# Kernel optimization log

Hardware: AMD Instinct MI355X
Metric: run time of the kernel (lower is better)

Reference implementation:

```python
import itertools
import jax, jax.numpy as jnp
import numpy as np

ALPHA = 1e-4   # mse/conn mixing
BETA = 0.1
DMAX = 20.0
NCAP = 10.0    # costs_n_cap
PCAP = 3.0     # costs_p_cap
W3D = 64       # 3D cube window (window_3d)
W2D = 32       # 2D MALIS window (window_2d, default)


def _dilate5(mask):
    # scipy binary_dilation, default cross structuring element, 5 iterations
    m = mask.astype(bool)
    for _ in range(5):
        p = np.pad(m, 1)
        m = p[1:-1, 1:-1] | p[:-2, 1:-1] | p[2:, 1:-1] | p[1:-1, :-2] | p[1:-1, 2:]
    return m


def _label8(mask):
    # skimage.measure.label on boolean mask: 8-connectivity, background=0
    H, W = mask.shape
    lbl = np.zeros((H, W), np.int64)
    parent = {}

    def find(x):
        while parent[x] != x:
            parent[x] = parent[parent[x]]
            x = parent[x]
        return x

    nxt = 1
    for i in range(H):
        for j in range(W):
            if not mask[i, j]:
                continue
            neigh = []
            for di, dj in ((-1, -1), (-1, 0), (-1, 1), (0, -1)):
                ii, jj = i + di, j + dj
                if 0 <= ii < H and 0 <= jj < W and mask[ii, jj]:
                    neigh.append(int(lbl[ii, jj]))
            if not neigh:
                lbl[i, j] = nxt
                parent[nxt] = nxt
                nxt += 1
            else:
                m0 = min(neigh)
                lbl[i, j] = m0
                for nb in neigh:
                    ra, rb = find(m0), find(nb)
                    if ra != rb:
                        parent[max(ra, rb)] = min(ra, rb)
    out = np.zeros_like(lbl)
    remap = {}
    c = 0
    for i in range(H):
        for j in range(W):
            if lbl[i, j] > 0:
                r = find(int(lbl[i, j]))
                if r not in remap:
                    c += 1
                    remap[r] = c
                out[i, j] = remap[r]
    return out


def _malis_edge_weights(seg, n1, n2, costs, pos):
    # MALIS union-find / Kruskal maximal-spanning-tree pair counting.
    # Edges processed in descending cost order. Background (seg==0) nodes
    # are not counted. pos=1: #same-label pairs merged; pos=0: #diff-label pairs.
    n = seg.size
    parent = list(range(n))

    def find(x):
        r = x
        while parent[r] != r:
            r = parent[r]
        while parent[x] != r:
            parent[x], x = r, parent[x]
        return r

    cnt = [({int(s): 1} if s > 0 else {}) for s in seg]
    tot = [1 if s > 0 else 0 for s in seg]
    w = np.zeros(costs.shape[0], np.float32)
    for e in np.argsort(-costs, kind="stable"):
        ra, rb = find(int(n1[e])), find(int(n2[e]))
        if ra == rb:
            continue
        ca, cb = cnt[ra], cnt[rb]
        if len(ca) > len(cb):
            ra, rb, ca, cb = rb, ra, cb, ca
        same = 0
        for l, v in ca.items():
            same += v * cb.get(l, 0)
        w[e] = float(same if pos else tot[ra] * tot[rb] - same)
        for l, v in ca.items():
            cb[l] = cb.get(l, 0) + v
        tot[rb] += tot[ra]
        parent[ra] = rb
        cnt[ra] = None
    return w


def _window_weights(pred2d, tgt2d):
    # numpy MALIS node weights for a [B,1,H,W] 2D projection
    B, C, H, W = pred2d.shape
    w = W2D
    wn = np.zeros(pred2d.shape, np.float32)
    wp = np.zeros(pred2d.shape, np.float32)
    idx = np.arange(w * w).reshape(w, w)
    n1 = np.concatenate([idx[:, :-1].ravel(), idx[:-1, :].ravel()])
    n2 = np.concatenate([idx[:, 1:].ravel(), idx[1:, :].ravel()])
    nh = w * (w - 1)
    for k in range(H // w):
        for j in range(W // w):
            p = pred2d[:, :, k*w:(k+1)*w, j*w:(j+1)*w]
            t = tgt2d[:, :, k*w:(k+1)*w, j*w:(j+1)*w]
            ch = (p[:, :, :, :-1] + p[:, :, :, 1:]).reshape(B, -1)
            cv = (p[:, :, :-1, :] + p[:, :, 1:, :]).reshape(B, -1)
            costs = np.concatenate([ch, cv], 1).astype(np.float32)
            gh = (t[:, :, :, :-1] + t[:, :, :, 1:]).reshape(B, -1)
            gv = (t[:, :, :-1, :] + t[:, :, 1:, :]).reshape(B, -1)
            gt = np.concatenate([gh, gv], 1).astype(np.float32)
            costs_n = costs.copy()
            costs_p = costs.copy()
            costs_n[gt > NCAP] = NCAP
            costs_p[gt < PCAP] = 0.0
            gt = np.minimum(gt, NCAP)
            for b in range(B):
                sg = _label8(~_dilate5(t[b, 0] == 0)).ravel()
                en = _malis_edge_weights(sg, n1, n2, costs_n[b], 0)
                ep = _malis_edge_weights(sg, n1, n2, costs_p[b], 1)
                sn = en.sum()
                if sn > 0:
                    en = en / sn
                sp = ep.sum()
                if sp > 0:
                    ep = ep / sp
                en[gt[b] >= PCAP] = 0.0
                ep[gt[b] < NCAP] = 0.0
                for ew, out in ((en, wn), (ep, wp)):
                    eh = ew[:nh].reshape(w, w - 1)
                    ev = ew[nh:].reshape(w - 1, w)
                    nwt = np.zeros((w, w), np.float32)
                    nwt[:, :-1] += eh
                    nwt[:, 1:] += eh
                    nwt[:-1, :] += ev
                    nwt[1:, :] += ev
                    out[b, 0, k*w:(k+1)*w, j*w:(j+1)*w] = nwt
    return wn, wp


def _precompute(pred_np, tgt_np):
    # host-side (detached) MALIS weight maps, exactly as the torch module
    B, C, H, W, D = pred_np.shape
    items = []
    for k, j, i in itertools.product(range(H // W3D), range(W // W3D), range(D // W3D)):
        sl = (slice(None), slice(None), slice(k*W3D, (k+1)*W3D),
              slice(j*W3D, (j+1)*W3D), slice(i*W3D, (i+1)*W3D))
        pc, tc = pred_np[sl], tgt_np[sl]
        for axis in (2, 3, 4):
            wn, wp = _window_weights(pc.min(axis=axis), tc.min(axis=axis))
            items.append((k, j, i, axis, jnp.asarray(wn), jnp.asarray(wp)))
    return items


def _loss(pred, target, items):
    mse = jnp.mean((pred - target) ** 2)
    conn = jnp.float32(0.0)
    for (k, j, i, axis, wn, wp) in items:
        pc = pred[:, :, k*W3D:(k+1)*W3D, j*W3D:(j+1)*W3D, i*W3D:(i+1)*W3D]
        proj = jnp.min(pc, axis=axis)  # [B,1,64,64]
        conn = conn + jnp.sum(proj**2 * wn + BETA * (DMAX - proj)**2 * wp)
    return (mse, jnp.float32(ALPHA) * conn)


def setup_inputs() -> dict:
    # synthetic distance-transform-like volumes (zeros on 'vessel' seeds)
    rng = np.random.default_rng(0)
    B, H = 4, 128
    g = np.arange(H, dtype=np.float32)
    zz, yy, xx = np.meshgrid(g, g, g, indexing="ij")
    tgt = np.empty((B, 1, H, H, H), np.float32)
    for b in range(B):
        pts = rng.uniform(0, H, size=(24, 3)).astype(np.float32)
        d = np.full((H, H, H), np.inf, np.float32)
        for p in pts:
            d = np.minimum(d, np.sqrt((zz - p[0])**2 + (yy - p[1])**2 + (xx - p[2])**2))
        tgt[b, 0] = np.floor(np.minimum(d, DMAX))
    pred = np.clip(tgt + 0.5 * rng.standard_normal(tgt.shape).astype(np.float32), 0.0, DMAX).astype(np.float32)
    return {"pred": jnp.asarray(pred), "target": jnp.asarray(tgt)}


def reference(pred, target):
    items = _precompute(np.asarray(pred), np.asarray(target))
    return _loss(pred, target, items)
```

## Files before the change

### kernel.cpp

```cpp
#include <hip/hip_runtime.h>

#define BLOCK 256
#define NNODE 1024
#define NH    992
#define NE    1984
#define NSORT 2048
#define LMAX  12
#define CHUNK 64
#define NPASS (NE / CHUNK)

typedef unsigned long long ull;

__device__ __forceinline__ void edge_nodes(int e, int& a, int& b) {
    if (e < NH) {
        int r = e / 31;
        int c = e - r * 31;
        a = (r << 5) + c;
        b = a + 1;
    } else {
        a = e - NH;
        b = a + 32;
    }
}

__device__ __forceinline__ int find_par(unsigned short* par, int x) {
    volatile unsigned short* vp = par;
    int r = x;
    int p = vp[r];
    while (p != r) { r = p; p = vp[r]; }
    int c = x;
    while (c != r) { const int nxt = vp[c]; vp[c] = (unsigned short)r; c = nxt; }
    return r;
}

__device__ __forceinline__ int dot16x4(ull a, ull b) {
    int s  = (int)(a & 0xFFFFu)         * (int)(b & 0xFFFFu);
    s     += (int)((a >> 16) & 0xFFFFu) * (int)((b >> 16) & 0xFFFFu);
    s     += (int)((a >> 32) & 0xFFFFu) * (int)((b >> 32) & 0xFFFFu);
    s     += (int)((a >> 48) & 0xFFFFu) * (int)((b >> 48) & 0xFFFFu);
    return s;
}

__device__ __forceinline__ void cswap(unsigned int& ka, unsigned short& ia,
                                      unsigned int& kb, unsigned short& ib, bool up) {
    const bool gt = (ka > kb) || (ka == kb && ia > ib);
    if (gt == up) {
        const unsigned int  tk = ka; ka = kb; kb = tk;
        const unsigned short ti = ia; ia = ib; ib = ti;
    }
}

template<int MODE>
__device__ __forceinline__ void kruskal_run(unsigned short* sh_parent,
                                            unsigned int*   sh_szto,
                                            ull*            sh_cnt64,
                                            unsigned int*   sh_key,
                                            const unsigned short* sh_idx,
                                            const int sign, const int lane) {
    unsigned int* claim32 = (unsigned int*)sh_cnt64;
    for (int pass = 0; pass < NPASS; ++pass) {
        const int e = sh_idx[pass * CHUNK + lane];
        int a, bb; edge_nodes(e, a, bb);
        int ra = find_par(sh_parent, a);
        int rb = find_par(sh_parent, bb);
        bool cand = (ra != rb);

        if (MODE <= 1) {
            const unsigned int tag = ((unsigned int)(pass + 1) << 6) | (unsigned int)(63 - lane);
            const int ia = (MODE == 0) ? ra : (ra * 6 + 2);
            const int ib = (MODE == 0) ? rb : (rb * 6 + 2);
            if (cand) {
                atomicMax(&claim32[ia], tag);
                atomicMax(&claim32[ib], tag);
            }
            asm volatile("s_waitcnt lgkmcnt(0)" ::: "memory");
            __builtin_amdgcn_sched_barrier(0);
            bool win = false;
            if (cand) win = (claim32[ia] == tag) && (claim32[ib] == tag);
            if (win) {
                const unsigned int xa = sh_szto[ra], xb = sh_szto[rb];
                const int ta = (int)(xa >> 16), tb = (int)(xb >> 16);
                int wv;
                ull a0 = 0, b0 = 0;
                if (MODE == 0) {
                    wv = ta * tb;
                } else {
                    a0 = sh_cnt64[ra * 3]; b0 = sh_cnt64[rb * 3];
                    const int same = dot16x4(a0, b0);
                    wv = sign ? same : (ta * tb - same);
                }
                const int big = ((xa & 0xFFFFu) > (xb & 0xFFFFu));
                const int rs = big ? ra : rb;
                const int rl = big ? rb : ra;
                sh_key[e] = __float_as_uint((float)wv);
                sh_szto[rs] = xa + xb;
                if (MODE == 1 && (ta + tb) > 0) sh_cnt64[rs * 3] = a0 + b0;
                sh_parent[rl] = (unsigned short)rs;
                cand = false;
            }
            asm volatile("s_waitcnt lgkmcnt(0)" ::: "memory");
            __builtin_amdgcn_sched_barrier(0);
            if (cand) {
                ra = find_par(sh_parent, ra);
                rb = find_par(sh_parent, rb);
                cand = (ra != rb);
            }
        }

        ull m = __ballot(cand);
        while (m) {
            const int i = (int)__builtin_ctzll(m);
            m &= m - 1;
            const unsigned int pack = (unsigned int)ra | ((unsigned int)rb << 10) | ((unsigned int)e << 20);
            const unsigned int pk = (unsigned int)__shfl((int)pack, i);
            const int ra_i = (int)(pk & 1023u);
            const int rb_i = (int)((pk >> 10) & 1023u);
            if (ra_i == rb_i) continue;
            const int se = (int)(pk >> 20);
            const unsigned int xa = sh_szto[ra_i], xb = sh_szto[rb_i];
            const int ta = (int)(xa >> 16), tb = (int)(xb >> 16);
            const int big = ((xa & 0xFFFFu) > (xb & 0xFFFFu));
            const int rs = big ? ra_i : rb_i;
            const int rl = big ? rb_i : ra_i;
            int wv;
            if (MODE == 0) {
                wv = ta * tb;
            } else if (MODE == 1) {
                const ull a0 = sh_cnt64[ra_i * 3];
                const ull b0 = sh_cnt64[rb_i * 3];
                const int same = dot16x4(a0, b0);
                wv = sign ? same : (ta * tb - same);
                if (lane == 0 && (ta + tb) > 0)
                    sh_cnt64[rs * 3] = a0 + b0;
            } else {
                const ull a0 = sh_cnt64[ra_i * 3 + 0];
                const ull a1 = sh_cnt64[ra_i * 3 + 1];
                const ull a2 = sh_cnt64[ra_i * 3 + 2];
                const ull b0 = sh_cnt64[rb_i * 3 + 0];
                const ull b1 = sh_cnt64[rb_i * 3 + 1];
                const ull b2 = sh_cnt64[rb_i * 3 + 2];
                const int same = dot16x4(a0, b0) + dot16x4(a1, b1) + dot16x4(a2, b2);
                wv = sign ? same : (ta * tb - same);
                if (lane == 0 && (ta + tb) > 0) {
                    sh_cnt64[rs * 3 + 0] = a0 + b0;
                    sh_cnt64[rs * 3 + 1] = a1 + b1;
                    sh_cnt64[rs * 3 + 2] = a2 + b2;
                }
            }
            if (lane == 0) {
                sh_key[se] = __float_as_uint((float)wv);
                sh_szto[rs] = xa + xb;
                sh_parent[rl] = (unsigned short)rs;
            }
            if (ra == rl) ra = rs;
            if (rb == rl) rb = rs;
        }
    }
}

template<int MODE>
__device__ __forceinline__ void uf_init(unsigned short* sh_parent,
                                        unsigned int* sh_szto,
                                        ull* sh_cnt64,
                                        const unsigned char* sh_seg,
                                        const int tid) {
    unsigned int* claim32 = (unsigned int*)sh_cnt64;
    for (int pix = tid; pix < NNODE; pix += BLOCK) {
        sh_parent[pix] = (unsigned short)pix;
        const int s = sh_seg[pix];
        const unsigned int tot = (s > 0 && s <= LMAX) ? 1u : 0u;
        sh_szto[pix] = 1u | (tot << 16);
        if (MODE == 0) {
            claim32[pix] = 0u;
        } else {
            ull c0 = 0, c1 = 0, c2 = 0;
            if (s >= 1 && s <= LMAX) {
                const ull bit = 1ull << (((s - 1) & 3) * 16);
                const int q = (s - 1) >> 2;
                if (q == 0) c0 = bit; else if (q == 1) c1 = bit; else c2 = bit;
            }
            sh_cnt64[pix * 3 + 0] = c0;
            sh_cnt64[pix * 3 + 1] = (MODE == 1) ? 0ull : c1;
            if (MODE == 2) sh_cnt64[pix * 3 + 2] = c2;
        }
    }
}

__global__ __launch_bounds__(BLOCK) void prep_kernel(const float* __restrict__ pred,
                                                     const float* __restrict__ tgt,
                                                     char* __restrict__ ws,
                                                     double* __restrict__ acc_ws,
                                                     int B) {
    __shared__ alignas(16) float sh_p[NNODE];
    __shared__ alignas(16) float sh_t[NNODE];
    __shared__ unsigned char  mA[NNODE];
    __shared__ unsigned char  mB[NNODE];
    __shared__ unsigned short sh_parent[NNODE];
    __shared__ unsigned short sh_lab[NNODE];
    __shared__ int sh_flag;
    __shared__ int sh_L;
    __shared__ double sh_redp[4];

    const int tid = threadIdx.x;
    const int w = blockIdx.x;
    int wg = w;
    const int b    = wg % B;  wg /= B;
    const int win  = wg & 3;  wg >>= 2;
    const int item = wg;
    const int axis_id = item % 3;
    const int cube = item / 3;
    const int ci = cube & 1;
    const int cj = (cube >> 1) & 1;
    const int ck = (cube >> 2) & 1;
    const int wk = win >> 1;
    const int wj = win & 1;

    const int NW = 96 * B;
    float* Pb = (float*)(ws + 64);
    float* Tb = Pb + (size_t)NW * NNODE;
    unsigned char* Sb = (unsigned char*)(Tb + (size_t)NW * NNODE);
    int* Lb = (int*)(Sb + (size_t)NW * NNODE);

    const size_t base = (size_t)b * 2097152u;

    if (axis_id == 2) {
        double msum = 0.0;
        for (int pix = tid; pix < NNODE; pix += BLOCK) {
            const int r = pix >> 5, c = pix & 31;
            const int R = wk * 32 + r, C = wj * 32 + c;
            const size_t idx0 = base + (size_t)(ck * 64 + R) * 16384u + (size_t)(cj * 64 + C) * 128u + (size_t)(ci * 64);
            const float4* pp = reinterpret_cast<const float4*>(pred + idx0);
            const float4* tp = reinterpret_cast<const float4*>(tgt + idx0);
            float pm = 3.4e38f, tm = 3.4e38f;
            #pragma unroll
            for (int h = 0; h < 16; ++h) {
                const float4 a = pp[h];
                const float4 t = tp[h];
                pm = fminf(pm, fminf(fminf(a.x, a.y), fminf(a.z, a.w)));
                tm = fminf(tm, fminf(fminf(t.x, t.y), fminf(t.z, t.w)));
                const float dx = a.x - t.x, dy = a.y - t.y;
                const float dz = a.z - t.z, dw = a.w - t.w;
                msum += (double)(dx * dx);
                msum += (double)(dy * dy);
                msum += (double)(dz * dz);
                msum += (double)(dw * dw);
            }
            sh_p[pix] = pm;
            sh_t[pix] = tm;
        }
        for (int off = 32; off > 0; off >>= 1) msum += __shfl_down(msum, off, 64);
        if ((tid & 63) == 0) sh_redp[tid >> 6] = msum;
        __syncthreads();
        if (tid == 0)
            atomicAdd(&acc_ws[0], sh_redp[0] + sh_redp[1] + sh_redp[2] + sh_redp[3]);
    } else {
        const int r  = tid >> 3;
        const int c0 = (tid & 7) << 2;
        const int R = wk * 32 + r, C = wj * 32 + c0;
        size_t idx0; int hstride;
        if (axis_id == 0) {
            idx0 = base + (size_t)(ck * 64) * 16384u + (size_t)(cj * 64 + R) * 128u + (size_t)(ci * 64 + C);
            hstride = 16384;
        } else {
            idx0 = base + (size_t)(ck * 64 + R) * 16384u + (size_t)(cj * 64) * 128u + (size_t)(ci * 64 + C);
            hstride = 128;
        }
        float4 pm = make_float4(3.4e38f, 3.4e38f, 3.4e38f, 3.4e38f);
        float4 tm = pm;
        #pragma unroll 8
        for (int h = 0; h < 64; ++h) {
            const float4 a  = *reinterpret_cast<const float4*>(pred + idx0);
            const float4 t4 = *reinterpret_cast<const float4*>(tgt + idx0);
            pm.x = fminf(pm.x, a.x);  pm.y = fminf(pm.y, a.y);
            pm.z = fminf(pm.z, a.z);  pm.w = fminf(pm.w, a.w);
            tm.x = fminf(tm.x, t4.x); tm.y = fminf(tm.y, t4.y);
            tm.z = fminf(tm.z, t4.z); tm.w = fminf(tm.w, t4.w);
            idx0 += (size_t)hstride;
        }
        *reinterpret_cast<float4*>(&sh_p[(r << 5) + c0]) = pm;
        *reinterpret_cast<float4*>(&sh_t[(r << 5) + c0]) = tm;
        __syncthreads();
    }

    for (int pix = tid; pix < NNODE; pix += BLOCK)
        mA[pix] = (sh_t[pix] == 0.0f) ? 1 : 0;
    __syncthreads();
    for (int it = 0; it < 5; ++it) {
        unsigned char* src = (it & 1) ? mB : mA;
        unsigned char* dst = (it & 1) ? mA : mB;
        for (int pix = tid; pix < NNODE; pix += BLOCK) {
            const int r = pix >> 5, c = pix & 31;
            unsigned char v = src[pix];
            if (r > 0)  v |= src[pix - 32];
            if (r < 31) v |= src[pix + 32];
            if (c > 0)  v |= src[pix - 1];
            if (c < 31) v |= src[pix + 1];
            dst[pix] = v;
        }
        __syncthreads();
    }
    for (int pix = tid; pix < NNODE; pix += BLOCK)
        mA[pix] = mB[pix] ^ 1;
    __syncthreads();

    for (int pix = tid; pix < NNODE; pix += BLOCK)
        sh_parent[pix] = mA[pix] ? (unsigned short)pix : (unsigned short)0xFFFF;
    __syncthreads();
    for (;;) {
        if (tid == 0) sh_flag = 0;
        __syncthreads();
        for (int pix = tid; pix < NNODE; pix += BLOCK) {
            if (!mA[pix]) continue;
            const int r = pix >> 5, c = pix & 31;
            int m = sh_parent[pix];
            #pragma unroll
            for (int d = 0; d < 8; ++d) {
                static const int dr[8] = {-1,-1,-1, 0, 0, 1, 1, 1};
                static const int dc[8] = {-1, 0, 1,-1, 1,-1, 0, 1};
                const int rr = r + dr[d], cc = c + dc[d];
                if (rr < 0 || rr > 31 || cc < 0 || cc > 31) continue;
                const int nb = (rr << 5) + cc;
                if (mA[nb]) { int v = sh_parent[nb]; if (v < m) m = v; }
            }
            while ((int)sh_parent[m] < m) m = sh_parent[m];
            if (m < (int)sh_parent[pix]) { sh_parent[pix] = (unsigned short)m; sh_flag = 1; }
        }
        __syncthreads();
        const int f = sh_flag;
        __syncthreads();
        if (f == 0) break;
    }

    if (tid == 0) sh_L = 0;
    __syncthreads();
    for (int pix = tid; pix < NNODE; pix += BLOCK) {
        if (mA[pix] && (int)sh_parent[pix] == pix) {
            const int id = atomicAdd(&sh_L, 1);
            sh_lab[pix] = (unsigned short)(id + 1);
        }
    }
    __syncthreads();

    {
        const int p4 = tid << 2;
        *reinterpret_cast<float4*>(&Pb[(size_t)w * NNODE + p4]) =
            *reinterpret_cast<const float4*>(&sh_p[p4]);
        *reinterpret_cast<float4*>(&Tb[(size_t)w * NNODE + p4]) =
            *reinterpret_cast<const float4*>(&sh_t[p4]);
        unsigned int packed = 0;
        #pragma unroll
        for (int q = 0; q < 4; ++q) {
            const int pix = p4 + q;
            unsigned int s = 0;
            if (mA[pix]) {
                int lab = sh_lab[sh_parent[pix]];
                if (lab > 255) lab = 255;
                s = (unsigned int)lab;
            }
            packed |= s << (q * 8);
        }
        ((unsigned int*)Sb)[(size_t)w * (NNODE / 4) + tid] = packed;
        if (tid == 0) Lb[w] = sh_L;
    }
}

__global__ __launch_bounds__(BLOCK) void solve_kernel(const char* __restrict__ ws_c,
                                                      double* __restrict__ acc_ws,
                                                      int B) {
    __shared__ alignas(16) float          sh_p[NNODE];
    __shared__ alignas(16) float          sh_t[NNODE];
    __shared__ alignas(16) unsigned int   sh_key[NSORT];
    __shared__ alignas(16) unsigned short sh_idx[NSORT];
    __shared__ unsigned short sh_parent[NNODE];
    __shared__ unsigned int   sh_szto[NNODE];
    __shared__ ull            sh_cnt64[NNODE * 3];
    __shared__ alignas(16) unsigned char sh_seg[NNODE];
    __shared__ float          sh_sn;
    __shared__ double         sh_red[4];

    const int tid = threadIdx.x;
    int wg = blockIdx.x;
    const int sign = wg & 1;  wg >>= 1;
    const int w = wg;

    const int NW = 96 * B;
    const float* Pb = (const float*)(ws_c + 64);
    const float* Tb = Pb + (size_t)NW * NNODE;
    const unsigned char* Sb = (const unsigned char*)(Tb + (size_t)NW * NNODE);
    const int* Lb = (const int*)(Sb + (size_t)NW * NNODE);

    const int Lraw = Lb[w];
    if (Lraw == 0 || (Lraw == 1 && sign == 0)) return;
    const int mode = (Lraw <= 1) ? 0 : ((Lraw <= 4) ? 1 : 2);

    {
        const int p4 = tid << 2;
        *reinterpret_cast<float4*>(&sh_p[p4]) =
            *reinterpret_cast<const float4*>(&Pb[(size_t)w * NNODE + p4]);
        *reinterpret_cast<float4*>(&sh_t[p4]) =
            *reinterpret_cast<const float4*>(&Tb[(size_t)w * NNODE + p4]);
        ((unsigned int*)sh_seg)[tid] =
            ((const unsigned int*)Sb)[(size_t)w * (NNODE / 4) + tid];
    }
    __syncthreads();

    if (mode == 0)      uf_init<0>(sh_parent, sh_szto, sh_cnt64, sh_seg, tid);
    else if (mode == 1) uf_init<1>(sh_parent, sh_szto, sh_cnt64, sh_seg, tid);
    else                uf_init<2>(sh_parent, sh_szto, sh_cnt64, sh_seg, tid);
    __syncthreads();

    unsigned int   K[8];
    unsigned short I[8];
    const int b8 = tid << 3;
    #pragma unroll
    for (int l = 0; l < 8; ++l) {
        const int e = b8 + l;
        if (e < NE) {
            int a, bb; edge_nodes(e, a, bb);
            float cost = sh_p[a] + sh_p[bb];
            const float g = sh_t[a] + sh_t[bb];
            if (sign == 0) { if (g > 10.0f) cost = 10.0f; }
            else           { if (g <  3.0f) cost = 0.0f;  }
            K[l] = ~__float_as_uint(cost);
            I[l] = (unsigned short)e;
        } else {
            K[l] = 0xFFFFFFFFu;
            I[l] = (unsigned short)0xFFFF;
        }
    }
    cswap(K[0],I[0],K[1],I[1], true );
    cswap(K[2],I[2],K[3],I[3], false);
    cswap(K[4],I[4],K[5],I[5], true );
    cswap(K[6],I[6],K[7],I[7], false);
    cswap(K[0],I[0],K[2],I[2], true );
    cswap(K[1],I[1],K[3],I[3], true );
    cswap(K[4],I[4],K[6],I[6], false);
    cswap(K[5],I[5],K[7],I[7], false);
    cswap(K[0],I[0],K[1],I[1], true );
    cswap(K[2],I[2],K[3],I[3], true );
    cswap(K[4],I[4],K[5],I[5], false);
    cswap(K[6],I[6],K[7],I[7], false);
    {
        const bool u8 = ((b8 & 8) == 0);
        cswap(K[0],I[0],K[4],I[4], u8); cswap(K[1],I[1],K[5],I[5], u8);
        cswap(K[2],I[2],K[6],I[6], u8); cswap(K[3],I[3],K[7],I[7], u8);
        cswap(K[0],I[0],K[2],I[2], u8); cswap(K[1],I[1],K[3],I[3], u8);
        cswap(K[4],I[4],K[6],I[6], u8); cswap(K[5],I[5],K[7],I[7], u8);
        cswap(K[0],I[0],K[1],I[1], u8); cswap(K[2],I[2],K[3],I[3], u8);
        cswap(K[4],I[4],K[5],I[5], u8); cswap(K[6],I[6],K[7],I[7], u8);
    }
    {
        uint4 k0, k1, iv;
        k0.x=K[0]; k0.y=K[1]; k0.z=K[2]; k0.w=K[3];
        k1.x=K[4]; k1.y=K[5]; k1.z=K[6]; k1.w=K[7];
        iv.x=(unsigned int)I[0] | ((unsigned int)I[1]<<16);
        iv.y=(unsigned int)I[2] | ((unsigned int)I[3]<<16);
        iv.z=(unsigned int)I[4] | ((unsigned int)I[5]<<16);
        iv.w=(unsigned int)I[6] | ((unsigned int)I[7]<<16);
        *reinterpret_cast<uint4*>(&sh_key[b8])     = k0;
        *reinterpret_cast<uint4*>(&sh_key[b8 + 4]) = k1;
        *reinterpret_cast<uint4*>(&sh_idx[b8])     = iv;
    }
    __syncthreads();

    for (int k = 16; k <= NSORT; k <<= 1) {
        for (int j = k >> 1; j >= 8; j >>= 1) {
            for (int p = tid; p < (NSORT >> 1); p += BLOCK) {
                const int i   = ((p & ~(j - 1)) << 1) | (p & (j - 1));
                const int ixj = i | j;
                const unsigned int ka = sh_key[i], kb = sh_key[ixj];
                const unsigned short ia = sh_idx[i], ib = sh_idx[ixj];
                const bool gt = (ka > kb) || (ka == kb && ia > ib);
                const bool up = ((i & k) == 0);
                if (gt == up) {
                    sh_key[i] = kb; sh_key[ixj] = ka;
                    sh_idx[i] = ib; sh_idx[ixj] = ia;
                }
            }
            __syncthreads();
        }
        {
            const uint4 k0 = *reinterpret_cast<const uint4*>(&sh_key[b8]);
            const uint4 k1 = *reinterpret_cast<const uint4*>(&sh_key[b8 + 4]);
            const uint4 iv = *reinterpret_cast<const uint4*>(&sh_idx[b8]);
            K[0]=k0.x; K[1]=k0.y; K[2]=k0.z; K[3]=k0.w;
            K[4]=k1.x; K[5]=k1.y; K[6]=k1.z; K[7]=k1.w;
            I[0]=(unsigned short)(iv.x); I[1]=(unsigned short)(iv.x>>16);
            I[2]=(unsigned short)(iv.y); I[3]=(unsigned short)(iv.y>>16);
            I[4]=(unsigned short)(iv.z); I[5]=(unsigned short)(iv.z>>16);
            I[6]=(unsigned short)(iv.w); I[7]=(unsigned short)(iv.w>>16);
            const bool u8 = ((b8 & k) == 0);
            cswap(K[0],I[0],K[4],I[4], u8); cswap(K[1],I[1],K[5],I[5], u8);
            cswap(K[2],I[2],K[6],I[6], u8); cswap(K[3],I[3],K[7],I[7], u8);
            cswap(K[0],I[0],K[2],I[2], u8); cswap(K[1],I[1],K[3],I[3], u8);
            cswap(K[4],I[4],K[6],I[6], u8); cswap(K[5],I[5],K[7],I[7], u8);
            cswap(K[0],I[0],K[1],I[1], u8); cswap(K[2],I[2],K[3],I[3], u8);
            cswap(K[4],I[4],K[5],I[5], u8); cswap(K[6],I[6],K[7],I[7], u8);
            uint4 o0, o1, ov;
            o0.x=K[0]; o0.y=K[1]; o0.z=K[2]; o0.w=K[3];
            o1.x=K[4]; o1.y=K[5]; o1.z=K[6]; o1.w=K[7];
            ov.x=(unsigned int)I[0] | ((unsigned int)I[1]<<16);
            ov.y=(unsigned int)I[2] | ((unsigned int)I[3]<<16);
            ov.z=(unsigned int)I[4] | ((unsigned int)I[5]<<16);
            ov.w=(unsigned int)I[6] | ((unsigned int)I[7]<<16);
            *reinterpret_cast<uint4*>(&sh_key[b8])     = o0;
            *reinterpret_cast<uint4*>(&sh_key[b8 + 4]) = o1;
            *reinterpret_cast<uint4*>(&sh_idx[b8])     = ov;
        }
        __syncthreads();
    }

    for (int e = tid; e < NE; e += BLOCK) sh_key[e] = 0u;
    __syncthreads();

    if (tid < 64) {
        if (mode == 0)      kruskal_run<0>(sh_parent, sh_szto, sh_cnt64, sh_key, sh_idx, sign, tid);
        else if (mode == 1) kruskal_run<1>(sh_parent, sh_szto, sh_cnt64, sh_key, sh_idx, sign, tid);
        else                kruskal_run<2>(sh_parent, sh_szto, sh_cnt64, sh_key, sh_idx, sign, tid);
    }
    __syncthreads();

    {
        float part = 0.0f;
        for (int e = tid; e < NE; e += BLOCK) part += __uint_as_float(sh_key[e]);
        for (int off = 32; off > 0; off >>= 1) part += __shfl_down(part, off, 64);
        if ((tid & 63) == 0) sh_red[tid >> 6] = (double)part;
        __syncthreads();
        if (tid == 0) sh_sn = (float)(sh_red[0] + sh_red[1] + sh_red[2] + sh_red[3]);
        __syncthreads();
    }
    const float sn = sh_sn;

    double acc = 0.0;
    for (int pix = tid; pix < NNODE; pix += BLOCK) {
        const int r = pix >> 5, c = pix & 31;
        float nw = 0.0f;
        if (c < 31) { const int e = r * 31 + c;
            float v = __uint_as_float(sh_key[e]); if (sn > 0.0f) v = v / sn;
            const float g = sh_t[pix] + sh_t[pix + 1];
            if (sign == 0) { if (g >= 3.0f) v = 0.0f; } else { if (g < 10.0f) v = 0.0f; }
            nw += v; }
        if (c > 0)  { const int e = r * 31 + c - 1;
            float v = __uint_as_float(sh_key[e]); if (sn > 0.0f) v = v / sn;
            const float g = sh_t[pix - 1] + sh_t[pix];
            if (sign == 0) { if (g >= 3.0f) v = 0.0f; } else { if (g < 10.0f) v = 0.0f; }
            nw += v; }
        if (r < 31) { const int e = NH + pix;
            float v = __uint_as_float(sh_key[e]); if (sn > 0.0f) v = v / sn;
            const float g = sh_t[pix] + sh_t[pix + 32];
            if (sign == 0) { if (g >= 3.0f) v = 0.0f; } else { if (g < 10.0f) v = 0.0f; }
            nw += v; }
        if (r > 0)  { const int e = NH + pix - 32;
            float v = __uint_as_float(sh_key[e]); if (sn > 0.0f) v = v / sn;
            const float g = sh_t[pix - 32] + sh_t[pix];
            if (sign == 0) { if (g >= 3.0f) v = 0.0f; } else { if (g < 10.0f) v = 0.0f; }
            nw += v; }
        const float p = sh_p[pix];
        float term;
        if (sign == 0) term = (p * p) * nw;
        else { const float d = 20.0f - p; term = (0.1f * (d * d)) * nw; }
        acc += (double)term;
    }
    for (int off = 32; off > 0; off >>= 1) acc += __shfl_down(acc, off, 64);
    if ((tid & 63) == 0) sh_red[tid >> 6] = acc;
    __syncthreads();
    if (tid == 0)
        atomicAdd(&acc_ws[1], sh_red[0] + sh_red[1] + sh_red[2] + sh_red[3]);
}

__global__ __launch_bounds__(BLOCK) void conn_kernel(const float* __restrict__ pred,
                                                     const float* __restrict__ tgt,
                                                     double* __restrict__ acc_ws,
                                                     int B) {
    __shared__ alignas(16) float          sh_p[NNODE];
    __shared__ alignas(16) float          sh_t[NNODE];
    __shared__ alignas(16) unsigned int   sh_key[NSORT];
    __shared__ alignas(16) unsigned short sh_idx[NSORT];
    __shared__ unsigned short sh_parent[NNODE];
    __shared__ unsigned int   sh_szto[NNODE];
    __shared__ ull            sh_cnt64[NNODE * 3];
    __shared__ unsigned char  sh_seg[NNODE];
    __shared__ int            sh_flag;
    __shared__ int            sh_L;
    __shared__ float          sh_sn;
    __shared__ double         sh_red[4];

    const int tid = threadIdx.x;
    int wg = blockIdx.x;
    const int sign = (wg >> 3) & 1;
    wg = (wg & 7) | ((wg >> 4) << 3);
    const int b    = wg % B;  wg /= B;
    const int win  = wg & 3;  wg >>= 2;
    const int item = wg;
    const int axis_id = item % 3;
    const int cube = item / 3;
    const int ci = cube & 1;
    const int cj = (cube >> 1) & 1;
    const int ck = (cube >> 2) & 1;
    const int wk = win >> 1;
    const int wj = win & 1;

    const size_t base = (size_t)b * 2097152u;

    if (axis_id == 2) {
        for (int pix = tid; pix < NNODE; pix += BLOCK) {
            const int r = pix >> 5, c = pix & 31;
            const int R = wk * 32 + r, C = wj * 32 + c;
            const size_t idx0 = base + (size_t)(ck * 64 + R) * 16384u + (size_t)(cj * 64 + C) * 128u + (size_t)(ci * 64);
            const float4* pp = reinterpret_cast<const float4*>(pred + idx0);
            const float4* tp = reinterpret_cast<const float4*>(tgt + idx0);
            float pm = 3.4e38f, tm = 3.4e38f;
            #pragma unroll
            for (int h = 0; h < 16; ++h) {
                const float4 a = pp[h];
                const float4 t = tp[h];
                pm = fminf(pm, fminf(fminf(a.x, a.y), fminf(a.z, a.w)));
                tm = fminf(tm, fminf(fminf(t.x, t.y), fminf(t.z, t.w)));
            }
            sh_p[pix] = pm;
            sh_t[pix] = tm;
        }
    } else {
        const int r  = tid >> 3;
        const int c0 = (tid & 7) << 2;
        const int R = wk * 32 + r, C = wj * 32 + c0;
        size_t idx0; int hstride;
        if (axis_id == 0) {
            idx0 = base + (size_t)(ck * 64) * 16384u + (size_t)(cj * 64 + R) * 128u + (size_t)(ci * 64 + C);
            hstride = 16384;
        } else {
            idx0 = base + (size_t)(ck * 64 + R) * 16384u + (size_t)(cj * 64) * 128u + (size_t)(ci * 64 + C);
            hstride = 128;
        }
        float4 pm = make_float4(3.4e38f, 3.4e38f, 3.4e38f, 3.4e38f);
        float4 tm = pm;
        #pragma unroll 8
        for (int h = 0; h < 64; ++h) {
            const float4 a  = *reinterpret_cast<const float4*>(pred + idx0);
            const float4 t4 = *reinterpret_cast<const float4*>(tgt + idx0);
            pm.x = fminf(pm.x, a.x);  pm.y = fminf(pm.y, a.y);
            pm.z = fminf(pm.z, a.z);  pm.w = fminf(pm.w, a.w);
            tm.x = fminf(tm.x, t4.x); tm.y = fminf(tm.y, t4.y);
            tm.z = fminf(tm.z, t4.z); tm.w = fminf(tm.w, t4.w);
            idx0 += (size_t)hstride;
        }
        *reinterpret_cast<float4*>(&sh_p[(r << 5) + c0]) = pm;
        *reinterpret_cast<float4*>(&sh_t[(r << 5) + c0]) = tm;
    }
    __syncthreads();

    unsigned char* mA = sh_seg;
    unsigned char* mB = (unsigned char*)sh_idx;
    for (int pix = tid; pix < NNODE; pix += BLOCK)
        mA[pix] = (sh_t[pix] == 0.0f) ? 1 : 0;
    __syncthreads();
    for (int it = 0; it < 5; ++it) {
        unsigned char* src = (it & 1) ? mB : mA;
        unsigned char* dst = (it & 1) ? mA : mB;
        for (int pix = tid; pix < NNODE; pix += BLOCK) {
            const int r = pix >> 5, c = pix & 31;
            unsigned char v = src[pix];
            if (r > 0)  v |= src[pix - 32];
            if (r < 31) v |= src[pix + 32];
            if (c > 0)  v |= src[pix - 1];
            if (c < 31) v |= src[pix + 1];
            dst[pix] = v;
        }
        __syncthreads();
    }
    for (int pix = tid; pix < NNODE; pix += BLOCK)
        mA[pix] = mB[pix] ^ 1;
    __syncthreads();

    for (int pix = tid; pix < NNODE; pix += BLOCK)
        sh_parent[pix] = mA[pix] ? (unsigned short)pix : (unsigned short)0xFFFF;
    __syncthreads();
    for (;;) {
        if (tid == 0) sh_flag = 0;
        __syncthreads();
        for (int pix = tid; pix < NNODE; pix += BLOCK) {
            if (!mA[pix]) continue;
            const int r = pix >> 5, c = pix & 31;
            int m = sh_parent[pix];
            #pragma unroll
            for (int d = 0; d < 8; ++d) {
                static const int dr[8] = {-1,-1,-1, 0, 0, 1, 1, 1};
                static const int dc[8] = {-1, 0, 1,-1, 1,-1, 0, 1};
                const int rr = r + dr[d], cc = c + dc[d];
                if (rr < 0 || rr > 31 || cc < 0 || cc > 31) continue;
                const int nb = (rr << 5) + cc;
                if (mA[nb]) { int v = sh_parent[nb]; if (v < m) m = v; }
            }
            while ((int)sh_parent[m] < m) m = sh_parent[m];
            if (m < (int)sh_parent[pix]) { sh_parent[pix] = (unsigned short)m; sh_flag = 1; }
        }
        __syncthreads();
        const int f = sh_flag;
        __syncthreads();
        if (f == 0) break;
    }

    if (tid == 0) sh_L = 0;
    __syncthreads();
    for (int pix = tid; pix < NNODE; pix += BLOCK) {
        if (mA[pix] && (int)sh_parent[pix] == pix) {
            const int id = atomicAdd(&sh_L, 1);
            sh_szto[pix] = (unsigned int)(id + 1);
        }
    }
    __syncthreads();
    for (int pix = tid; pix < NNODE; pix += BLOCK) {
        unsigned char s = 0;
        if (mA[pix]) {
            int lab = (int)sh_szto[sh_parent[pix]];
            if (lab > 255) lab = 255;
            s = (unsigned char)lab;
        }
        sh_seg[pix] = s;
    }
    __syncthreads();

    const int Lraw = sh_L;
    const int mode = (Lraw <= 1) ? 0 : ((Lraw <= 4) ? 1 : 2);
    const bool skip_all = (Lraw == 0) || (Lraw == 1 && sign == 0);

    if (!skip_all) {

    if (mode == 0)      uf_init<0>(sh_parent, sh_szto, sh_cnt64, sh_seg, tid);
    else if (mode == 1) uf_init<1>(sh_parent, sh_szto, sh_cnt64, sh_seg, tid);
    else                uf_init<2>(sh_parent, sh_szto, sh_cnt64, sh_seg, tid);
    __syncthreads();

    unsigned int   K[8];
    unsigned short I[8];
    const int b8 = tid << 3;
    #pragma unroll
    for (int l = 0; l < 8; ++l) {
        const int e = b8 + l;
        if (e < NE) {
            int a, bb; edge_nodes(e, a, bb);
            float cost = sh_p[a] + sh_p[bb];
            const float g = sh_t[a] + sh_t[bb];
            if (sign == 0) { if (g > 10.0f) cost = 10.0f; }
            else           { if (g <  3.0f) cost = 0.0f;  }
            K[l] = ~__float_as_uint(cost);
            I[l] = (unsigned short)e;
        } else {
            K[l] = 0xFFFFFFFFu;
            I[l] = (unsigned short)0xFFFF;
        }
    }
    cswap(K[0],I[0],K[1],I[1], true );
    cswap(K[2],I[2],K[3],I[3], false);
    cswap(K[4],I[4],K[5],I[5], true );
    cswap(K[6],I[6],K[7],I[7], false);
    cswap(K[0],I[0],K[2],I[2], true );
    cswap(K[1],I[1],K[3],I[3], true );
    cswap(K[4],I[4],K[6],I[6], false);
    cswap(K[5],I[5],K[7],I[7], false);
    cswap(K[0],I[0],K[1],I[1], true );
    cswap(K[2],I[2],K[3],I[3], true );
    cswap(K[4],I[4],K[5],I[5], false);
    cswap(K[6],I[6],K[7],I[7], false);
    {
        const bool u8 = ((b8 & 8) == 0);
        cswap(K[0],I[0],K[4],I[4], u8); cswap(K[1],I[1],K[5],I[5], u8);
        cswap(K[2],I[2],K[6],I[6], u8); cswap(K[3],I[3],K[7],I[7], u8);
        cswap(K[0],I[0],K[2],I[2], u8); cswap(K[1],I[1],K[3],I[3], u8);
        cswap(K[4],I[4],K[6],I[6], u8); cswap(K[5],I[5],K[7],I[7], u8);
        cswap(K[0],I[0],K[1],I[1], u8); cswap(K[2],I[2],K[3],I[3], u8);
        cswap(K[4],I[4],K[5],I[5], u8); cswap(K[6],I[6],K[7],I[7], u8);
    }
    {
        uint4 k0, k1, iv;
        k0.x=K[0]; k0.y=K[1]; k0.z=K[2]; k0.w=K[3];
        k1.x=K[4]; k1.y=K[5]; k1.z=K[6]; k1.w=K[7];
        iv.x=(unsigned int)I[0] | ((unsigned int)I[1]<<16);
        iv.y=(unsigned int)I[2] | ((unsigned int)I[3]<<16);
        iv.z=(unsigned int)I[4] | ((unsigned int)I[5]<<16);
        iv.w=(unsigned int)I[6] | ((unsigned int)I[7]<<16);
        *reinterpret_cast<uint4*>(&sh_key[b8])     = k0;
        *reinterpret_cast<uint4*>(&sh_key[b8 + 4]) = k1;
        *reinterpret_cast<uint4*>(&sh_idx[b8])     = iv;
    }
    __syncthreads();

    for (int k = 16; k <= NSORT; k <<= 1) {
        for (int j = k >> 1; j >= 8; j >>= 1) {
            for (int p = tid; p < (NSORT >> 1); p += BLOCK) {
                const int i   = ((p & ~(j - 1)) << 1) | (p & (j - 1));
                const int ixj = i | j;
                const unsigned int ka = sh_key[i], kb = sh_key[ixj];
                const unsigned short ia = sh_idx[i], ib = sh_idx[ixj];
                const bool gt = (ka > kb) || (ka == kb && ia > ib);
                const bool up = ((i & k) == 0);
                if (gt == up) {
                    sh_key[i] = kb; sh_key[ixj] = ka;
                    sh_idx[i] = ib; sh_idx[ixj] = ia;
                }
            }
            __syncthreads();
        }
        {
            const uint4 k0 = *reinterpret_cast<const uint4*>(&sh_key[b8]);
            const uint4 k1 = *reinterpret_cast<const uint4*>(&sh_key[b8 + 4]);
            const uint4 iv = *reinterpret_cast<const uint4*>(&sh_idx[b8]);
            K[0]=k0.x; K[1]=k0.y; K[2]=k0.z; K[3]=k0.w;
            K[4]=k1.x; K[5]=k1.y; K[6]=k1.z; K[7]=k1.w;
            I[0]=(unsigned short)(iv.x); I[1]=(unsigned short)(iv.x>>16);
            I[2]=(unsigned short)(iv.y); I[3]=(unsigned short)(iv.y>>16);
            I[4]=(unsigned short)(iv.z); I[5]=(unsigned short)(iv.z>>16);
            I[6]=(unsigned short)(iv.w); I[7]=(unsigned short)(iv.w>>16);
            const bool u8 = ((b8 & k) == 0);
            cswap(K[0],I[0],K[4],I[4], u8); cswap(K[1],I[1],K[5],I[5], u8);
            cswap(K[2],I[2],K[6],I[6], u8); cswap(K[3],I[3],K[7],I[7], u8);
            cswap(K[0],I[0],K[2],I[2], u8); cswap(K[1],I[1],K[3],I[3], u8);
            cswap(K[4],I[4],K[6],I[6], u8); cswap(K[5],I[5],K[7],I[7], u8);
            cswap(K[0],I[0],K[1],I[1], u8); cswap(K[2],I[2],K[3],I[3], u8);
            cswap(K[4],I[4],K[5],I[5], u8); cswap(K[6],I[6],K[7],I[7], u8);
            uint4 o0, o1, ov;
            o0.x=K[0]; o0.y=K[1]; o0.z=K[2]; o0.w=K[3];
            o1.x=K[4]; o1.y=K[5]; o1.z=K[6]; o1.w=K[7];
            ov.x=(unsigned int)I[0] | ((unsigned int)I[1]<<16);
            ov.y=(unsigned int)I[2] | ((unsigned int)I[3]<<16);
            ov.z=(unsigned int)I[4] | ((unsigned int)I[5]<<16);
            ov.w=(unsigned int)I[6] | ((unsigned int)I[7]<<16);
            *reinterpret_cast<uint4*>(&sh_key[b8])     = o0;
            *reinterpret_cast<uint4*>(&sh_key[b8 + 4]) = o1;
            *reinterpret_cast<uint4*>(&sh_idx[b8])     = ov;
        }
        __syncthreads();
    }

    for (int e = tid; e < NE; e += BLOCK) sh_key[e] = 0u;
    __syncthreads();

    if (tid < 64) {
        if (mode == 0)      kruskal_run<0>(sh_parent, sh_szto, sh_cnt64, sh_key, sh_idx, sign, tid);
        else if (mode == 1) kruskal_run<1>(sh_parent, sh_szto, sh_cnt64, sh_key, sh_idx, sign, tid);
        else                kruskal_run<2>(sh_parent, sh_szto, sh_cnt64, sh_key, sh_idx, sign, tid);
    }
    __syncthreads();

    {
        float part = 0.0f;
        for (int e = tid; e < NE; e += BLOCK) part += __uint_as_float(sh_key[e]);
        for (int off = 32; off > 0; off >>= 1) part += __shfl_down(part, off, 64);
        if ((tid & 63) == 0) sh_red[tid >> 6] = (double)part;
        __syncthreads();
        if (tid == 0) sh_sn = (float)(sh_red[0] + sh_red[1] + sh_red[2] + sh_red[3]);
        __syncthreads();
    }
    const float sn = sh_sn;

    double acc = 0.0;
    for (int pix = tid; pix < NNODE; pix += BLOCK) {
        const int r = pix >> 5, c = pix & 31;
        float nw = 0.0f;
        if (c < 31) { const int e = r * 31 + c;
            float v = __uint_as_float(sh_key[e]); if (sn > 0.0f) v = v / sn;
            const float g = sh_t[pix] + sh_t[pix + 1];
            if (sign == 0) { if (g >= 3.0f) v = 0.0f; } else { if (g < 10.0f) v = 0.0f; }
            nw += v; }
        if (c > 0)  { const int e = r * 31 + c - 1;
            float v = __uint_as_float(sh_key[e]); if (sn > 0.0f) v = v / sn;
            const float g = sh_t[pix - 1] + sh_t[pix];
            if (sign == 0) { if (g >= 3.0f) v = 0.0f; } else { if (g < 10.0f) v = 0.0f; }
            nw += v; }
        if (r < 31) { const int e = NH + pix;
            float v = __uint_as_float(sh_key[e]); if (sn > 0.0f) v = v / sn;
            const float g = sh_t[pix] + sh_t[pix + 32];
            if (sign == 0) { if (g >= 3.0f) v = 0.0f; } else { if (g < 10.0f) v = 0.0f; }
            nw += v; }
        if (r > 0)  { const int e = NH + pix - 32;
            float v = __uint_as_float(sh_key[e]); if (sn > 0.0f) v = v / sn;
            const float g = sh_t[pix - 32] + sh_t[pix];
            if (sign == 0) { if (g >= 3.0f) v = 0.0f; } else { if (g < 10.0f) v = 0.0f; }
            nw += v; }
        const float p = sh_p[pix];
        float term;
        if (sign == 0) term = (p * p) * nw;
        else { const float d = 20.0f - p; term = (0.1f * (d * d)) * nw; }
        acc += (double)term;
    }
    for (int off = 32; off > 0; off >>= 1) acc += __shfl_down(acc, off, 64);
    if ((tid & 63) == 0) sh_red[tid >> 6] = acc;
    __syncthreads();
    if (tid == 0)
        atomicAdd(&acc_ws[1], sh_red[0] + sh_red[1] + sh_red[2] + sh_red[3]);

    }
}

__global__ __launch_bounds__(BLOCK) void mse_kernel(const float* __restrict__ pred,
                                                    const float* __restrict__ tgt,
                                                    double* __restrict__ acc_ws,
                                                    long n) {
    double acc = 0.0;
    for (long i = (long)blockIdx.x * BLOCK + threadIdx.x; i < n; i += (long)gridDim.x * BLOCK) {
        const float d = pred[i] - tgt[i];
        acc += (double)(d * d);
    }
    for (int off = 32; off > 0; off >>= 1) acc += __shfl_down(acc, off, 64);
    __shared__ double red[4];
    if ((threadIdx.x & 63) == 0) red[threadIdx.x >> 6] = acc;
    __syncthreads();
    if (threadIdx.x == 0)
        atomicAdd(&acc_ws[0], red[0] + red[1] + red[2] + red[3]);
}

__global__ void fin_kernel(const double* __restrict__ acc_ws, float* __restrict__ out, long n) {
    if (threadIdx.x == 0 && blockIdx.x == 0) {
        out[0] = (float)(acc_ws[0] / (double)n);
        out[1] = (float)(acc_ws[1] * (double)1e-4f);
    }
}

extern "C" void kernel_launch(void* const* d_in, const int* in_sizes, int n_in,
                              void* d_out, int out_size, void* d_ws, size_t ws_size,
                              hipStream_t stream) {
    const float* pred = (const float*)d_in[0];
    const float* tgt  = (const float*)d_in[1];
    float* out = (float*)d_out;
    double* acc = (double*)d_ws;

    const long n = (long)in_sizes[0];
    const int  B = (int)(n / 2097152);
    const int  NW = 96 * B;
    const size_t need = 64 + (size_t)NW * NNODE * 9 + (size_t)NW * 4;

    hipMemsetAsync(d_ws, 0, 2 * sizeof(double), stream);
    if (ws_size >= need) {
        prep_kernel<<<NW, BLOCK, 0, stream>>>(pred, tgt, (char*)d_ws, acc, B);
        solve_kernel<<<192 * B, BLOCK, 0, stream>>>((const char*)d_ws, acc, B);
    } else {
        mse_kernel<<<1024, BLOCK, 0, stream>>>(pred, tgt, acc, n);
        conn_kernel<<<192 * B, BLOCK, 0, stream>>>(pred, tgt, acc, B);
    }
    fin_kernel<<<1, 64, 0, stream>>>(acc, out, n);
}
```

Baseline: 473.4 us.

## Extend parallel claim-based Kruskal merging to more label counts with repeated rounds

The parallel atomicMax claim phase of the wave-level Kruskal pass now also runs for windows with up to 8 labels, using the spare third slot of each node's count array as the claim word. It also repeats the claim/merge step up to three rounds per 64-edge chunk, stopping early once fewer than 10 candidates remain. A new mode 3 keeps the old fully serial path for windows with more than 8 labels. The aim is to shrink the serial ballot loop, which handles one merge per iteration. The cost is extra atomics, LDS traffic and find calls per round, and more template instantiations.

```diff
diff --git a/kernel.cpp b/kernel.cpp
--- a/kernel.cpp
+++ b/kernel.cpp
@@ -65,45 +65,57 @@
         int rb = find_par(sh_parent, bb);
         bool cand = (ra != rb);
 
-        if (MODE <= 1) {
-            const unsigned int tag = ((unsigned int)(pass + 1) << 6) | (unsigned int)(63 - lane);
-            const int ia = (MODE == 0) ? ra : (ra * 6 + 2);
-            const int ib = (MODE == 0) ? rb : (rb * 6 + 2);
-            if (cand) {
-                atomicMax(&claim32[ia], tag);
-                atomicMax(&claim32[ib], tag);
-            }
-            asm volatile("s_waitcnt lgkmcnt(0)" ::: "memory");
-            __builtin_amdgcn_sched_barrier(0);
-            bool win = false;
-            if (cand) win = (claim32[ia] == tag) && (claim32[ib] == tag);
-            if (win) {
-                const unsigned int xa = sh_szto[ra], xb = sh_szto[rb];
-                const int ta = (int)(xa >> 16), tb = (int)(xb >> 16);
-                int wv;
-                ull a0 = 0, b0 = 0;
-                if (MODE == 0) {
-                    wv = ta * tb;
-                } else {
-                    a0 = sh_cnt64[ra * 3]; b0 = sh_cnt64[rb * 3];
-                    const int same = dot16x4(a0, b0);
-                    wv = sign ? same : (ta * tb - same);
+        if (MODE < 3) {
+            for (int round = 0; round < 3; ++round) {
+                const unsigned int tag =
+                    ((unsigned int)(pass * 4 + round + 1) << 6) | (unsigned int)(63 - lane);
+                const int ia = ra * 6 + 2 * MODE;
+                const int ib = rb * 6 + 2 * MODE;
+                if (cand) {
+                    atomicMax(&claim32[ia], tag);
+                    atomicMax(&claim32[ib], tag);
                 }
-                const int big = ((xa & 0xFFFFu) > (xb & 0xFFFFu));
-                const int rs = big ? ra : rb;
-                const int rl = big ? rb : ra;
-                sh_key[e] = __float_as_uint((float)wv);
-                sh_szto[rs] = xa + xb;
-                if (MODE == 1 && (ta + tb) > 0) sh_cnt64[rs * 3] = a0 + b0;
-                sh_parent[rl] = (unsigned short)rs;
-                cand = false;
-            }
-            asm volatile("s_waitcnt lgkmcnt(0)" ::: "memory");
-            __builtin_amdgcn_sched_barrier(0);
-            if (cand) {
-                ra = find_par(sh_parent, ra);
-                rb = find_par(sh_parent, rb);
-                cand = (ra != rb);
+                asm volatile("s_waitcnt lgkmcnt(0)" ::: "memory");
+                __builtin_amdgcn_sched_barrier(0);
+                bool win = false;
+                if (cand) win = (claim32[ia] == tag) && (claim32[ib] == tag);
+                if (win) {
+                    const unsigned int xa = sh_szto[ra], xb = sh_szto[rb];
+                    const int ta = (int)(xa >> 16), tb = (int)(xb >> 16);
+                    int wv;
+                    ull a0 = 0, a1 = 0, b0 = 0, b1 = 0;
+                    if (MODE == 0) {
+                        wv = ta * tb;
+                    } else {
+                        a0 = sh_cnt64[ra * 3]; b0 = sh_cnt64[rb * 3];
+                        int same = dot16x4(a0, b0);
+                        if (MODE >= 2) {
+                            a1 = sh_cnt64[ra * 3 + 1]; b1 = sh_cnt64[rb * 3 + 1];
+                            same += dot16x4(a1, b1);
+                        }
+                        wv = sign ? same : (ta * tb - same);
+                    }
+                    const int big = ((xa & 0xFFFFu) > (xb & 0xFFFFu));
+                    const int rs = big ? ra : rb;
+                    const int rl = big ? rb : ra;
+                    sh_key[e] = __float_as_uint((float)wv);
+                    sh_szto[rs] = xa + xb;
+                    if (MODE >= 1 && (ta + tb) > 0) {
+                        sh_cnt64[rs * 3] = a0 + b0;
+                        if (MODE >= 2) sh_cnt64[rs * 3 + 1] = a1 + b1;
+                    }
+                    sh_parent[rl] = (unsigned short)rs;
+                    cand = false;
+                }
+                asm volatile("s_waitcnt lgkmcnt(0)" ::: "memory");
+                __builtin_amdgcn_sched_barrier(0);
+                if (cand) {
+                    ra = find_par(sh_parent, ra);
+                    rb = find_par(sh_parent, rb);
+                    cand = (ra != rb);
+                }
+                const ull P = __ballot(cand);
+                if (__popcll(P) < 10) break;
             }
         }
 
@@ -125,26 +137,24 @@
             int wv;
             if (MODE == 0) {
                 wv = ta * tb;
-            } else if (MODE == 1) {
-                const ull a0 = sh_cnt64[ra_i * 3];
-                const ull b0 = sh_cnt64[rb_i * 3];
-                const int same = dot16x4(a0, b0);
-                wv = sign ? same : (ta * tb - same);
-                if (lane == 0 && (ta + tb) > 0)
-                    sh_cnt64[rs * 3] = a0 + b0;
             } else {
                 const ull a0 = sh_cnt64[ra_i * 3 + 0];
-                const ull a1 = sh_cnt64[ra_i * 3 + 1];
-                const ull a2 = sh_cnt64[ra_i * 3 + 2];
                 const ull b0 = sh_cnt64[rb_i * 3 + 0];
-                const ull b1 = sh_cnt64[rb_i * 3 + 1];
-                const ull b2 = sh_cnt64[rb_i * 3 + 2];
-                const int same = dot16x4(a0, b0) + dot16x4(a1, b1) + dot16x4(a2, b2);
+                ull a1 = 0, a2 = 0, b1 = 0, b2 = 0;
+                int same = dot16x4(a0, b0);
+                if (MODE >= 2) {
+                    a1 = sh_cnt64[ra_i * 3 + 1]; b1 = sh_cnt64[rb_i * 3 + 1];
+                    same += dot16x4(a1, b1);
+                }
+                if (MODE >= 3) {
+                    a2 = sh_cnt64[ra_i * 3 + 2]; b2 = sh_cnt64[rb_i * 3 + 2];
+                    same += dot16x4(a2, b2);
+                }
                 wv = sign ? same : (ta * tb - same);
                 if (lane == 0 && (ta + tb) > 0) {
                     sh_cnt64[rs * 3 + 0] = a0 + b0;
-                    sh_cnt64[rs * 3 + 1] = a1 + b1;
-                    sh_cnt64[rs * 3 + 2] = a2 + b2;
+                    if (MODE >= 2) sh_cnt64[rs * 3 + 1] = a1 + b1;
+                    if (MODE >= 3) sh_cnt64[rs * 3 + 2] = a2 + b2;
                 }
             }
             if (lane == 0) {
@@ -164,24 +174,30 @@
                                         ull* sh_cnt64,
                                         const unsigned char* sh_seg,
                                         const int tid) {
-    unsigned int* claim32 = (unsigned int*)sh_cnt64;
     for (int pix = tid; pix < NNODE; pix += BLOCK) {
         sh_parent[pix] = (unsigned short)pix;
         const int s = sh_seg[pix];
         const unsigned int tot = (s > 0 && s <= LMAX) ? 1u : 0u;
         sh_szto[pix] = 1u | (tot << 16);
+        ull c0 = 0, c1 = 0, c2 = 0;
+        if (s >= 1 && s <= LMAX) {
+            const ull bit = 1ull << (((s - 1) & 3) * 16);
+            const int q = (s - 1) >> 2;
+            if (q == 0) c0 = bit; else if (q == 1) c1 = bit; else c2 = bit;
+        }
         if (MODE == 0) {
-            claim32[pix] = 0u;
+            sh_cnt64[pix * 3 + 0] = 0ull;
+        } else if (MODE == 1) {
+            sh_cnt64[pix * 3 + 0] = c0;
+            sh_cnt64[pix * 3 + 1] = 0ull;
+        } else if (MODE == 2) {
+            sh_cnt64[pix * 3 + 0] = c0;
+            sh_cnt64[pix * 3 + 1] = c1;
+            sh_cnt64[pix * 3 + 2] = 0ull;
         } else {
-            ull c0 = 0, c1 = 0, c2 = 0;
-            if (s >= 1 && s <= LMAX) {
-                const ull bit = 1ull << (((s - 1) & 3) * 16);
-                const int q = (s - 1) >> 2;
-                if (q == 0) c0 = bit; else if (q == 1) c1 = bit; else c2 = bit;
-            }
             sh_cnt64[pix * 3 + 0] = c0;
-            sh_cnt64[pix * 3 + 1] = (MODE == 1) ? 0ull : c1;
-            if (MODE == 2) sh_cnt64[pix * 3 + 2] = c2;
+            sh_cnt64[pix * 3 + 1] = c1;
+            sh_cnt64[pix * 3 + 2] = c2;
         }
     }
 }
@@ -391,7 +407,7 @@
 
     const int Lraw = Lb[w];
     if (Lraw == 0 || (Lraw == 1 && sign == 0)) return;
-    const int mode = (Lraw <= 1) ? 0 : ((Lraw <= 4) ? 1 : 2);
+    const int mode = (Lraw <= 1) ? 0 : ((Lraw <= 4) ? 1 : ((Lraw <= 8) ? 2 : 3));
 
     {
         const int p4 = tid << 2;
@@ -406,7 +422,8 @@
 
     if (mode == 0)      uf_init<0>(sh_parent, sh_szto, sh_cnt64, sh_seg, tid);
     else if (mode == 1) uf_init<1>(sh_parent, sh_szto, sh_cnt64, sh_seg, tid);
-    else                uf_init<2>(sh_parent, sh_szto, sh_cnt64, sh_seg, tid);
+    else if (mode == 2) uf_init<2>(sh_parent, sh_szto, sh_cnt64, sh_seg, tid);
+    else                uf_init<3>(sh_parent, sh_szto, sh_cnt64, sh_seg, tid);
     __syncthreads();
 
     unsigned int   K[8];
@@ -516,7 +533,8 @@
     if (tid < 64) {
         if (mode == 0)      kruskal_run<0>(sh_parent, sh_szto, sh_cnt64, sh_key, sh_idx, sign, tid);
         else if (mode == 1) kruskal_run<1>(sh_parent, sh_szto, sh_cnt64, sh_key, sh_idx, sign, tid);
-        else                kruskal_run<2>(sh_parent, sh_szto, sh_cnt64, sh_key, sh_idx, sign, tid);
+        else if (mode == 2) kruskal_run<2>(sh_parent, sh_szto, sh_cnt64, sh_key, sh_idx, sign, tid);
+        else                kruskal_run<3>(sh_parent, sh_szto, sh_cnt64, sh_key, sh_idx, sign, tid);
     }
     __syncthreads();
 
@@ -721,14 +739,15 @@
     __syncthreads();
 
     const int Lraw = sh_L;
-    const int mode = (Lraw <= 1) ? 0 : ((Lraw <= 4) ? 1 : 2);
+    const int mode = (Lraw <= 1) ? 0 : ((Lraw <= 4) ? 1 : ((Lraw <= 8) ? 2 : 3));
     const bool skip_all = (Lraw == 0) || (Lraw == 1 && sign == 0);
 
     if (!skip_all) {
 
     if (mode == 0)      uf_init<0>(sh_parent, sh_szto, sh_cnt64, sh_seg, tid);
     else if (mode == 1) uf_init<1>(sh_parent, sh_szto, sh_cnt64, sh_seg, tid);
-    else                uf_init<2>(sh_parent, sh_szto, sh_cnt64, sh_seg, tid);
+    else if (mode == 2) uf_init<2>(sh_parent, sh_szto, sh_cnt64, sh_seg, tid);
+    else                uf_init<3>(sh_parent, sh_szto, sh_cnt64, sh_seg, tid);
     __syncthreads();
 
     unsigned int   K[8];
@@ -838,7 +857,8 @@
     if (tid < 64) {
         if (mode == 0)      kruskal_run<0>(sh_parent, sh_szto, sh_cnt64, sh_key, sh_idx, sign, tid);
         else if (mode == 1) kruskal_run<1>(sh_parent, sh_szto, sh_cnt64, sh_key, sh_idx, sign, tid);
-        else                kruskal_run<2>(sh_parent, sh_szto, sh_cnt64, sh_key, sh_idx, sign, tid);
+        else if (mode == 2) kruskal_run<2>(sh_parent, sh_szto, sh_cnt64, sh_key, sh_idx, sign, tid);
+        else                kruskal_run<3>(sh_parent, sh_szto, sh_cnt64, sh_key, sh_idx, sign, tid);
     }
     __syncthreads();
 
```

New measurement: 483.8 us. +2.2%, slower.
